# Kernel optimization log

Measured on AMD Instinct MI355X. Metric: run time of the kernel, lower is better.

Reference implementation:

```python
import jax, jax.numpy as jnp
import numpy as np

NX = 128      # number of sequential layers (columns)
NY = 1024     # active state width
NYPAD = 1024
B = 256       # batch of state vectors


def _banded_weights(key):
    """Tridiagonal weight stack [NX, NYPAD, NYPAD] matching torch init.

    Torch init: for layers l < NX-1, weight[y, y]=0.1, weight[y-1, y]=0.01,
    weight[y+1, y]=0.01 for y in [0, NY); last layer is all zero. To mimic a
    trained (non-degenerate) state while preserving the banded connection
    structure, we add small noise on the band positions of every layer.
    """
    d = jnp.zeros(NYPAD).at[:NY].set(0.1)
    u = jnp.zeros(NYPAD - 1).at[:NY - 1].set(0.01)
    base = jnp.diag(d) + jnp.diag(u, 1) + jnp.diag(u, -1)   # [NYPAD, NYPAD]
    band_mask = (base > 0).astype(jnp.float32)
    noise = 0.01 * jax.random.normal(key, (NX, NYPAD, NYPAD), dtype=jnp.float32)
    return (base[None, :, :] + noise) * band_mask[None, :, :]


def setup_inputs() -> dict:
    key = jax.random.key(0)
    kx, kw = jax.random.split(key)
    x = jax.random.normal(kx, (B, NYPAD), dtype=jnp.float32)
    W = _banded_weights(kw)  # [NX, NYPAD, NYPAD]
    return {"x": x, "W": W}


def reference(x, W):
    # forward: x = layer(x) for each layer; torch Linear is x @ weight.T
    def step(h, w):
        return h @ w.T, None
    out, _ = jax.lax.scan(step, x, W)
    return out
```

## Files before the change

kernel.cpp:

```cpp
#include <hip/hip_runtime.h>
#include <hip/hip_bf16.h>


#define NXL 128
#define NYP 1024
#define NB  256
#define NQ  32
#define SL  128
#define HR  136

struct __attribute__((packed, aligned(4))) f4u { float x, y, z, w; };

__global__ __launch_bounds__(256) void gather_compose(const float* __restrict__ W,
                                                      __hip_bfloat16* __restrict__ band9) {
    __shared__ float ta[4][3][HR];
    const int blk = blockIdx.x;
    const int q   = blk >> 3;
    const int s   = blk & 7;
    const int i0  = s * SL;
    const int tid = threadIdx.x;

#pragma unroll
    for (int g = tid; g < 4 * HR; g += 256) {
        int ly = g / HR;
        int rr = g - ly * HR;
        int i  = i0 - 4 + rr;
        float a = 0.0f, b = 0.0f, c = 0.0f;
        if ((unsigned)i < NYP) {
            size_t base = ((size_t)(4 * q + ly) << 20) + (size_t)i * (NYP + 1);
            const float* lp = W + base + ((i == 0) ? 0 : (i == NYP - 1) ? -3 : -1);
            f4u v = *reinterpret_cast<const f4u*>(lp);
            if (i == 0)            { a = 0.0f; b = v.x; c = v.y; }
            else if (i == NYP - 1) { a = v.z;  b = v.w; c = 0.0f; }
            else                   { a = v.x;  b = v.y; c = v.z; }
        }
        ta[ly][0][rr] = a;
        ta[ly][1][rr] = b;
        ta[ly][2][rr] = c;
    }
    __syncthreads();

    if (tid < SL) {
        const int i  = i0 + tid;
        const int li = tid + 4;
        float p[11], r[11];
#pragma unroll
        for (int k = 0; k < 11; ++k) { p[k] = 0.0f; r[k] = 0.0f; }
        p[4] = ta[3][0][li]; p[5] = ta[3][1][li]; p[6] = ta[3][2][li];

#pragma unroll
        for (int d = -2; d <= 2; ++d)
            r[d + 5] = fmaf(p[d + 6], ta[2][0][li + d + 1],
                       fmaf(p[d + 5], ta[2][1][li + d],
                            p[d + 4] * ta[2][2][li + d - 1]));
#pragma unroll
        for (int k = 0; k < 11; ++k) p[k] = r[k];

#pragma unroll
        for (int d = -3; d <= 3; ++d)
            r[d + 5] = fmaf(p[d + 6], ta[1][0][li + d + 1],
                       fmaf(p[d + 5], ta[1][1][li + d],
                            p[d + 4] * ta[1][2][li + d - 1]));
#pragma unroll
        for (int k = 0; k < 11; ++k) p[k] = r[k];

#pragma unroll
        for (int d = -4; d <= 4; ++d)
            r[d + 5] = fmaf(p[d + 6], ta[0][0][li + d + 1],
                       fmaf(p[d + 5], ta[0][1][li + d],
                            p[d + 4] * ta[0][2][li + d - 1]));

        __hip_bfloat16* dst = band9 + (size_t)q * 9 * NYP + i;
#pragma unroll
        for (int d = 0; d < 9; ++d)
            dst[d * NYP] = __float2bfloat16(r[d + 1]);
    }
}

struct B9u { uint2 d[9]; };

__device__ __forceinline__ void load9(const __hip_bfloat16* __restrict__ band9,
                                      int q, int r0, B9u& w) {
    const __hip_bfloat16* base = band9 + (size_t)q * 9 * NYP + r0;
#pragma unroll
    for (int d = 0; d < 9; ++d)
        w.d[d] = *reinterpret_cast<const uint2*>(base + d * NYP);
}

__device__ __forceinline__ float blo(unsigned u) { return __uint_as_float(u << 16); }
__device__ __forceinline__ float bhi(unsigned u) { return __uint_as_float(u & 0xffff0000u); }

__device__ __forceinline__ float wc(const B9u& w, int d, int j) {
    unsigned u = (j < 2) ? w.d[d].x : w.d[d].y;
    return (j & 1) ? bhi(u) : blo(u);
}

__device__ __forceinline__ void step9(float (&h)[4], const B9u& w,
                                      float (&hLds)[4], float (&hRds)[4],
                                      float (*nxt)[2][4], int wv, int lane) {
    float hl[4], hr[4];
#pragma unroll
    for (int j = 0; j < 4; ++j) {
        float su = __shfl_up(h[j], 1);
        float sd = __shfl_down(h[j], 1);
        hl[j] = (lane == 0)  ? hLds[j] : su;
        hr[j] = (lane == 63) ? hRds[j] : sd;
    }
    float n[4];
#pragma unroll
    for (int j = 0; j < 4; ++j) {
        float acc = 0.0f;
#pragma unroll
        for (int d = 0; d < 9; ++d)
            if (j + d >= 4 && j + d <= 7) acc = fmaf(wc(w, d, j), h[j + d - 4], acc);
#pragma unroll
        for (int d = 0; d < 9; ++d)
            if (j + d < 4) acc = fmaf(wc(w, d, j), hl[j + d], acc);
#pragma unroll
        for (int d = 0; d < 9; ++d)
            if (j + d > 7) acc = fmaf(wc(w, d, j), hr[j + d - 8], acc);
        n[j] = acc;
    }
#pragma unroll
    for (int j = 0; j < 4; ++j) h[j] = n[j];
    if (lane == 0) {
#pragma unroll
        for (int j = 0; j < 4; ++j) nxt[wv][0][j] = h[j];
    }
    if (lane == 63) {
#pragma unroll
        for (int j = 0; j < 4; ++j) nxt[wv][1][j] = h[j];
    }
    asm volatile("s_waitcnt lgkmcnt(0)" ::: "memory");
    __builtin_amdgcn_s_barrier();
#pragma unroll
    for (int j = 0; j < 4; ++j) {
        hLds[j] = nxt[(wv + 3) & 3][1][j];
        hRds[j] = nxt[(wv + 1) & 3][0][j];
    }
}

__global__ __launch_bounds__(256) void propagate9(const float* __restrict__ x,
                                                  const __hip_bfloat16* __restrict__ band9,
                                                  float* __restrict__ out) {
    __shared__ float hal[2][4][2][4];
    const int b    = blockIdx.x;
    const int tid  = threadIdx.x;
    const int wv   = tid >> 6;
    const int lane = tid & 63;
    const int r0   = tid * 4;

    float h[4];
    {
        float4 v = *reinterpret_cast<const float4*>(x + (size_t)b * NYP + r0);
        h[0] = v.x; h[1] = v.y; h[2] = v.z; h[3] = v.w;
    }

    B9u WA, WB;
    load9(band9, 0, r0, WA);

    if (lane == 0) {
#pragma unroll
        for (int j = 0; j < 4; ++j) hal[0][wv][0][j] = h[j];
    }
    if (lane == 63) {
#pragma unroll
        for (int j = 0; j < 4; ++j) hal[0][wv][1][j] = h[j];
    }
    asm volatile("s_waitcnt lgkmcnt(0)" ::: "memory");
    __builtin_amdgcn_s_barrier();
    float hLds[4], hRds[4];
#pragma unroll
    for (int j = 0; j < 4; ++j) {
        hLds[j] = hal[0][(wv + 3) & 3][1][j];
        hRds[j] = hal[0][(wv + 1) & 3][0][j];
    }

#pragma unroll 1
    for (int s = 0; s < NQ; s += 2) {
        load9(band9, (s + 1 < NQ) ? s + 1 : NQ - 1, r0, WB);
        step9(h, WA, hLds, hRds, hal[1], wv, lane);
        load9(band9, (s + 2 < NQ) ? s + 2 : NQ - 1, r0, WA);
        step9(h, WB, hLds, hRds, hal[0], wv, lane);
    }

    *reinterpret_cast<float4*>(out + (size_t)b * NYP + r0) =
        make_float4(h[0], h[1], h[2], h[3]);
}

__device__ __forceinline__ float gAw(const float* __restrict__ Wl, int r) {
    return (r >= 1 && r < NYP) ? Wl[(size_t)r * NYP + (r - 1)] : 0.0f;
}
__device__ __forceinline__ float gBw(const float* __restrict__ Wl, int r) {
    return ((unsigned)r < NYP) ? Wl[(size_t)r * NYP + r] : 0.0f;
}
__device__ __forceinline__ float gCw(const float* __restrict__ Wl, int r) {
    return (r >= 0 && r < NYP - 1) ? Wl[(size_t)r * NYP + (r + 1)] : 0.0f;
}

struct W4 { float4 a, b, c; };

__device__ __forceinline__ void lds_barrier() {
    asm volatile("s_waitcnt lgkmcnt(0)" ::: "memory");
    __builtin_amdgcn_s_barrier();
}

__device__ __forceinline__ void layer_step(float (&h)[4], const W4& w,
                                           float (*cur)[2], float (*nxt)[2],
                                           int wv, int lane) {
    float ldsL = cur[(wv + 3) & 3][1];
    float ldsR = cur[(wv + 1) & 3][0];
    float left  = __shfl_up(h[3], 1);
    float right = __shfl_down(h[0], 1);
    if (lane == 0)  left  = ldsL;
    if (lane == 63) right = ldsR;
    float n0 = fmaf(w.a.x, left, fmaf(w.b.x, h[0], w.c.x * h[1]));
    float n1 = fmaf(w.a.y, h[0], fmaf(w.b.y, h[1], w.c.y * h[2]));
    float n2 = fmaf(w.a.z, h[1], fmaf(w.b.z, h[2], w.c.z * h[3]));
    float n3 = fmaf(w.a.w, h[2], fmaf(w.b.w, h[3], w.c.w * right));
    h[0] = n0; h[1] = n1; h[2] = n2; h[3] = n3;
    if (lane == 0)  nxt[wv][0] = h[0];
    if (lane == 63) nxt[wv][1] = h[3];
    lds_barrier();
}

__global__ __launch_bounds__(256) void propagate_direct(const float* __restrict__ x,
                                                        const float* __restrict__ W,
                                                        float* __restrict__ out) {
    __shared__ float hal[2][4][2];
    const int b    = blockIdx.x;
    const int tid  = threadIdx.x;
    const int wv   = tid >> 6;
    const int lane = tid & 63;
    const int r0   = tid * 4;

    float h[4];
    {
        float4 v = *reinterpret_cast<const float4*>(x + (size_t)b * NYP + r0);
        h[0] = v.x; h[1] = v.y; h[2] = v.z; h[3] = v.w;
    }

    if (lane == 0)  hal[0][wv][0] = h[0];
    if (lane == 63) hal[0][wv][1] = h[3];
    lds_barrier();

#pragma unroll 1
    for (int l = 0; l < NXL; ++l) {
        W4 w;
        float t0[4], t1[4], t2[4];
        const float* Wl = W + ((size_t)l << 20);
#pragma unroll
        for (int k = 0; k < 4; ++k) {
            int i = r0 + k;
            t0[k] = gAw(Wl, i); t1[k] = gBw(Wl, i); t2[k] = gCw(Wl, i);
        }
        w.a = make_float4(t0[0], t0[1], t0[2], t0[3]);
        w.b = make_float4(t1[0], t1[1], t1[2], t1[3]);
        w.c = make_float4(t2[0], t2[1], t2[2], t2[3]);
        if (l & 1) layer_step(h, w, hal[1], hal[0], wv, lane);
        else       layer_step(h, w, hal[0], hal[1], wv, lane);
    }

    *reinterpret_cast<float4*>(out + (size_t)b * NYP + r0) =
        make_float4(h[0], h[1], h[2], h[3]);
}

extern "C" void kernel_launch(void* const* d_in, const int* in_sizes, int n_in,
                              void* d_out, int out_size, void* d_ws, size_t ws_size,
                              hipStream_t stream) {
    const float* x = (const float*)d_in[0];
    const float* W = (const float*)d_in[1];
    float* out = (float*)d_out;

    const size_t band9Bytes = (size_t)NQ * 9 * NYP * sizeof(__hip_bfloat16);
    if (ws_size >= band9Bytes) {
        __hip_bfloat16* band9 = (__hip_bfloat16*)d_ws;
        gather_compose<<<NQ * 8, 256, 0, stream>>>(W, band9);
        propagate9<<<NB, 256, 0, stream>>>(x, band9, out);
    } else {
        propagate_direct<<<NB, 256, 0, stream>>>(x, W, out);
    }
}
```

Before: 29.47 us.

## Run each batch row in a single wavefront with 16 rows per lane

After: 53.87 us. 82.8% more time.

```diff
diff --git a/kernel.cpp b/kernel.cpp
--- a/kernel.cpp
+++ b/kernel.cpp
@@ -77,115 +77,82 @@
     }
 }
 
-struct B9u { uint2 d[9]; };
-
-__device__ __forceinline__ void load9(const __hip_bfloat16* __restrict__ band9,
-                                      int q, int r0, B9u& w) {
-    const __hip_bfloat16* base = band9 + (size_t)q * 9 * NYP + r0;
-#pragma unroll
-    for (int d = 0; d < 9; ++d)
-        w.d[d] = *reinterpret_cast<const uint2*>(base + d * NYP);
-}
-
 __device__ __forceinline__ float blo(unsigned u) { return __uint_as_float(u << 16); }
 __device__ __forceinline__ float bhi(unsigned u) { return __uint_as_float(u & 0xffff0000u); }
 
-__device__ __forceinline__ float wc(const B9u& w, int d, int j) {
-    unsigned u = (j < 2) ? w.d[d].x : w.d[d].y;
-    return (j & 1) ? bhi(u) : blo(u);
-}
-
-__device__ __forceinline__ void step9(float (&h)[4], const B9u& w,
-                                      float (&hLds)[4], float (&hRds)[4],
-                                      float (*nxt)[2][4], int wv, int lane) {
-    float hl[4], hr[4];
-#pragma unroll
-    for (int j = 0; j < 4; ++j) {
-        float su = __shfl_up(h[j], 1);
-        float sd = __shfl_down(h[j], 1);
-        hl[j] = (lane == 0)  ? hLds[j] : su;
-        hr[j] = (lane == 63) ? hRds[j] : sd;
-    }
-    float n[4];
-#pragma unroll
-    for (int j = 0; j < 4; ++j) {
+struct QW { uint4 u[18]; };
+
+__device__ __forceinline__ void loadQ(const __hip_bfloat16* __restrict__ band9,
+                                      int q, int r0, QW& w) {
+    const __hip_bfloat16* base = band9 + (size_t)q * 9 * NYP + r0;
+#pragma unroll
+    for (int d = 0; d < 9; ++d) {
+        w.u[2 * d]     = *reinterpret_cast<const uint4*>(base + d * NYP);
+        w.u[2 * d + 1] = *reinterpret_cast<const uint4*>(base + d * NYP + 8);
+    }
+}
+
+__device__ __forceinline__ float getw(const QW& w, int d, int j) {
+    const uint4& u = w.u[2 * d + (j >> 3)];
+    int k = (j >> 1) & 3;
+    unsigned v = (k == 0) ? u.x : (k == 1) ? u.y : (k == 2) ? u.z : u.w;
+    return (j & 1) ? bhi(v) : blo(v);
+}
+
+__device__ __forceinline__ void stepW(float (&h)[16], const QW& w) {
+    float lh[4], rh[4];
+#pragma unroll
+    for (int t = 0; t < 4; ++t) {
+        lh[t] = __shfl_up(h[12 + t], 1);
+        rh[t] = __shfl_down(h[t], 1);
+    }
+    float n[16];
+#pragma unroll
+    for (int j = 0; j < 16; ++j) {
         float acc = 0.0f;
 #pragma unroll
-        for (int d = 0; d < 9; ++d)
-            if (j + d >= 4 && j + d <= 7) acc = fmaf(wc(w, d, j), h[j + d - 4], acc);
-#pragma unroll
-        for (int d = 0; d < 9; ++d)
-            if (j + d < 4) acc = fmaf(wc(w, d, j), hl[j + d], acc);
-#pragma unroll
-        for (int d = 0; d < 9; ++d)
-            if (j + d > 7) acc = fmaf(wc(w, d, j), hr[j + d - 8], acc);
+        for (int d = 0; d < 9; ++d) {
+            int e = j + d - 4;
+            float hv = (e < 0) ? lh[e + 4] : (e > 15) ? rh[e - 16] : h[e];
+            acc = fmaf(getw(w, d, j), hv, acc);
+        }
         n[j] = acc;
     }
 #pragma unroll
-    for (int j = 0; j < 4; ++j) h[j] = n[j];
-    if (lane == 0) {
-#pragma unroll
-        for (int j = 0; j < 4; ++j) nxt[wv][0][j] = h[j];
-    }
-    if (lane == 63) {
-#pragma unroll
-        for (int j = 0; j < 4; ++j) nxt[wv][1][j] = h[j];
-    }
-    asm volatile("s_waitcnt lgkmcnt(0)" ::: "memory");
-    __builtin_amdgcn_s_barrier();
-#pragma unroll
-    for (int j = 0; j < 4; ++j) {
-        hLds[j] = nxt[(wv + 3) & 3][1][j];
-        hRds[j] = nxt[(wv + 1) & 3][0][j];
-    }
-}
-
-__global__ __launch_bounds__(256) void propagate9(const float* __restrict__ x,
+    for (int j = 0; j < 16; ++j) h[j] = n[j];
+}
+
+__global__ __launch_bounds__(64) void propagate9w(const float* __restrict__ x,
                                                   const __hip_bfloat16* __restrict__ band9,
                                                   float* __restrict__ out) {
-    __shared__ float hal[2][4][2][4];
     const int b    = blockIdx.x;
-    const int tid  = threadIdx.x;
-    const int wv   = tid >> 6;
-    const int lane = tid & 63;
-    const int r0   = tid * 4;
-
-    float h[4];
-    {
-        float4 v = *reinterpret_cast<const float4*>(x + (size_t)b * NYP + r0);
-        h[0] = v.x; h[1] = v.y; h[2] = v.z; h[3] = v.w;
-    }
-
-    B9u WA, WB;
-    load9(band9, 0, r0, WA);
-
-    if (lane == 0) {
-#pragma unroll
-        for (int j = 0; j < 4; ++j) hal[0][wv][0][j] = h[j];
-    }
-    if (lane == 63) {
-#pragma unroll
-        for (int j = 0; j < 4; ++j) hal[0][wv][1][j] = h[j];
-    }
-    asm volatile("s_waitcnt lgkmcnt(0)" ::: "memory");
-    __builtin_amdgcn_s_barrier();
-    float hLds[4], hRds[4];
-#pragma unroll
-    for (int j = 0; j < 4; ++j) {
-        hLds[j] = hal[0][(wv + 3) & 3][1][j];
-        hRds[j] = hal[0][(wv + 1) & 3][0][j];
-    }
+    const int lane = threadIdx.x & 63;
+    const int r0   = lane * 16;
+
+    float h[16];
+    const float4* xb = reinterpret_cast<const float4*>(x + (size_t)b * NYP + r0);
+#pragma unroll
+    for (int t = 0; t < 4; ++t) {
+        float4 v = xb[t];
+        h[4 * t + 0] = v.x; h[4 * t + 1] = v.y;
+        h[4 * t + 2] = v.z; h[4 * t + 3] = v.w;
+    }
+
+    QW QA, QB;
+    loadQ(band9, 0, r0, QA);
 
 #pragma unroll 1
     for (int s = 0; s < NQ; s += 2) {
-        load9(band9, (s + 1 < NQ) ? s + 1 : NQ - 1, r0, WB);
-        step9(h, WA, hLds, hRds, hal[1], wv, lane);
-        load9(band9, (s + 2 < NQ) ? s + 2 : NQ - 1, r0, WA);
-        step9(h, WB, hLds, hRds, hal[0], wv, lane);
-    }
-
-    *reinterpret_cast<float4*>(out + (size_t)b * NYP + r0) =
-        make_float4(h[0], h[1], h[2], h[3]);
+        loadQ(band9, (s + 1 < NQ) ? s + 1 : NQ - 1, r0, QB);
+        stepW(h, QA);
+        loadQ(band9, (s + 2 < NQ) ? s + 2 : NQ - 1, r0, QA);
+        stepW(h, QB);
+    }
+
+    float4* ob = reinterpret_cast<float4*>(out + (size_t)b * NYP + r0);
+#pragma unroll
+    for (int t = 0; t < 4; ++t)
+        ob[t] = make_float4(h[4 * t + 0], h[4 * t + 1], h[4 * t + 2], h[4 * t + 3]);
 }
 
 __device__ __forceinline__ float gAw(const float* __restrict__ Wl, int r) {
@@ -198,71 +165,49 @@
     return (r >= 0 && r < NYP - 1) ? Wl[(size_t)r * NYP + (r + 1)] : 0.0f;
 }
 
-struct W4 { float4 a, b, c; };
-
-__device__ __forceinline__ void lds_barrier() {
-    asm volatile("s_waitcnt lgkmcnt(0)" ::: "memory");
-    __builtin_amdgcn_s_barrier();
-}
-
-__device__ __forceinline__ void layer_step(float (&h)[4], const W4& w,
-                                           float (*cur)[2], float (*nxt)[2],
-                                           int wv, int lane) {
-    float ldsL = cur[(wv + 3) & 3][1];
-    float ldsR = cur[(wv + 1) & 3][0];
-    float left  = __shfl_up(h[3], 1);
-    float right = __shfl_down(h[0], 1);
-    if (lane == 0)  left  = ldsL;
-    if (lane == 63) right = ldsR;
-    float n0 = fmaf(w.a.x, left, fmaf(w.b.x, h[0], w.c.x * h[1]));
-    float n1 = fmaf(w.a.y, h[0], fmaf(w.b.y, h[1], w.c.y * h[2]));
-    float n2 = fmaf(w.a.z, h[1], fmaf(w.b.z, h[2], w.c.z * h[3]));
-    float n3 = fmaf(w.a.w, h[2], fmaf(w.b.w, h[3], w.c.w * right));
-    h[0] = n0; h[1] = n1; h[2] = n2; h[3] = n3;
-    if (lane == 0)  nxt[wv][0] = h[0];
-    if (lane == 63) nxt[wv][1] = h[3];
-    lds_barrier();
-}
-
-__global__ __launch_bounds__(256) void propagate_direct(const float* __restrict__ x,
-                                                        const float* __restrict__ W,
-                                                        float* __restrict__ out) {
-    __shared__ float hal[2][4][2];
+__global__ __launch_bounds__(64) void propagate_direct(const float* __restrict__ x,
+                                                       const float* __restrict__ W,
+                                                       float* __restrict__ out) {
     const int b    = blockIdx.x;
-    const int tid  = threadIdx.x;
-    const int wv   = tid >> 6;
-    const int lane = tid & 63;
-    const int r0   = tid * 4;
-
-    float h[4];
-    {
-        float4 v = *reinterpret_cast<const float4*>(x + (size_t)b * NYP + r0);
-        h[0] = v.x; h[1] = v.y; h[2] = v.z; h[3] = v.w;
-    }
-
-    if (lane == 0)  hal[0][wv][0] = h[0];
-    if (lane == 63) hal[0][wv][1] = h[3];
-    lds_barrier();
+    const int lane = threadIdx.x & 63;
+    const int r0   = lane * 16;
+
+    float h[16];
+    const float4* xb = reinterpret_cast<const float4*>(x + (size_t)b * NYP + r0);
+#pragma unroll
+    for (int t = 0; t < 4; ++t) {
+        float4 v = xb[t];
+        h[4 * t + 0] = v.x; h[4 * t + 1] = v.y;
+        h[4 * t + 2] = v.z; h[4 * t + 3] = v.w;
+    }
 
 #pragma unroll 1
     for (int l = 0; l < NXL; ++l) {
-        W4 w;
-        float t0[4], t1[4], t2[4];
         const float* Wl = W + ((size_t)l << 20);
-#pragma unroll
-        for (int k = 0; k < 4; ++k) {
+        float a[16], bb[16], c[16];
+#pragma unroll
+        for (int k = 0; k < 16; ++k) {
             int i = r0 + k;
-            t0[k] = gAw(Wl, i); t1[k] = gBw(Wl, i); t2[k] = gCw(Wl, i);
-        }
-        w.a = make_float4(t0[0], t0[1], t0[2], t0[3]);
-        w.b = make_float4(t1[0], t1[1], t1[2], t1[3]);
-        w.c = make_float4(t2[0], t2[1], t2[2], t2[3]);
-        if (l & 1) layer_step(h, w, hal[1], hal[0], wv, lane);
-        else       layer_step(h, w, hal[0], hal[1], wv, lane);
-    }
-
-    *reinterpret_cast<float4*>(out + (size_t)b * NYP + r0) =
-        make_float4(h[0], h[1], h[2], h[3]);
+            a[k] = gAw(Wl, i); bb[k] = gBw(Wl, i); c[k] = gCw(Wl, i);
+        }
+        float left  = __shfl_up(h[15], 1);
+        float right = __shfl_down(h[0], 1);
+        float carry = left;
+        float n[16];
+#pragma unroll
+        for (int j = 0; j < 16; ++j) {
+            float hp = (j == 15) ? right : h[j + 1];
+            n[j] = fmaf(a[j], carry, fmaf(bb[j], h[j], c[j] * hp));
+            carry = h[j];
+        }
+#pragma unroll
+        for (int j = 0; j < 16; ++j) h[j] = n[j];
+    }
+
+    float4* ob = reinterpret_cast<float4*>(out + (size_t)b * NYP + r0);
+#pragma unroll
+    for (int t = 0; t < 4; ++t)
+        ob[t] = make_float4(h[4 * t + 0], h[4 * t + 1], h[4 * t + 2], h[4 * t + 3]);
 }
 
 extern "C" void kernel_launch(void* const* d_in, const int* in_sizes, int n_in,
@@ -276,8 +221,8 @@
     if (ws_size >= band9Bytes) {
         __hip_bfloat16* band9 = (__hip_bfloat16*)d_ws;
         gather_compose<<<NQ * 8, 256, 0, stream>>>(W, band9);
-        propagate9<<<NB, 256, 0, stream>>>(x, band9, out);
+        propagate9w<<<NB, 64, 0, stream>>>(x, band9, out);
     } else {
-        propagate_direct<<<NB, 256, 0, stream>>>(x, W, out);
-    }
-}
+        propagate_direct<<<NB, 64, 0, stream>>>(x, W, out);
+    }
+}
```
